# Performance work log

Measured on AMD Instinct MI355X. Metric: run time of the kernel, lower is better.

## Reference

```python
import jax, jax.numpy as jnp
import numpy as np
from jax import lax

B, L, DM, NL = 2, 1024, 768, 4
E = 2 * DM          # d_inner
N = 16              # d_state
K = 4               # d_conv
R = DM // 16        # dt_rank = 48


def setup_inputs() -> dict:
    key = jax.random.key(0)
    ks = jax.random.split(key, 16)
    s = 0.02
    x = jax.random.normal(ks[0], (B, L, DM), jnp.float32)
    boundary_prob = jax.random.uniform(ks[1], (B, L, 1), jnp.float32)
    in_proj_w = jax.random.normal(ks[2], (NL, 2 * E, DM), jnp.float32) * s
    conv_w = jax.random.normal(ks[3], (NL, E, K), jnp.float32) * 0.3
    conv_b = jax.random.normal(ks[4], (NL, E), jnp.float32) * 0.02
    x_proj_w = jax.random.normal(ks[5], (NL, R + 2 * N, E), jnp.float32) * s
    dt_proj_w = jax.random.normal(ks[6], (NL, E, R), jnp.float32) * (R ** -0.5)
    dt_proj_b = jax.random.uniform(ks[7], (NL, E), jnp.float32, -4.6, -3.0)
    A_log = jnp.log(jnp.broadcast_to(jnp.arange(1, N + 1, dtype=jnp.float32), (NL, E, N)))
    ssm_D = jnp.ones((NL, E), jnp.float32)
    out_proj_w = jax.random.normal(ks[8], (NL, DM, E), jnp.float32) * s
    ln_w = jnp.ones((NL, DM), jnp.float32)
    ln_b = jnp.zeros((NL, DM), jnp.float32)
    normf_w = jnp.ones((DM,), jnp.float32)
    normf_b = jnp.zeros((DM,), jnp.float32)
    ctrl_w1 = jax.random.normal(ks[9], (DM, DM + 1), jnp.float32) * s
    ctrl_b1 = jnp.zeros((DM,), jnp.float32)
    ctrl_w2 = jax.random.normal(ks[10], (DM, DM), jnp.float32) * s
    ctrl_b2 = jnp.zeros((DM,), jnp.float32)
    out_ln_w = jnp.ones((DM,), jnp.float32)
    out_ln_b = jnp.zeros((DM,), jnp.float32)
    return dict(x=x, boundary_prob=boundary_prob, in_proj_w=in_proj_w, conv_w=conv_w,
                conv_b=conv_b, x_proj_w=x_proj_w, dt_proj_w=dt_proj_w, dt_proj_b=dt_proj_b,
                A_log=A_log, ssm_D=ssm_D, out_proj_w=out_proj_w, ln_w=ln_w, ln_b=ln_b,
                normf_w=normf_w, normf_b=normf_b, ctrl_w1=ctrl_w1, ctrl_b1=ctrl_b1,
                ctrl_w2=ctrl_w2, ctrl_b2=ctrl_b2, out_ln_w=out_ln_w, out_ln_b=out_ln_b)


def _layernorm(h, w, b):
    m = h.mean(-1, keepdims=True)
    v = ((h - m) ** 2).mean(-1, keepdims=True)
    return (h - m) * lax.rsqrt(v + 1e-5) * w + b


def reference(x, boundary_prob, in_proj_w, conv_w, conv_b, x_proj_w, dt_proj_w, dt_proj_b,
              A_log, ssm_D, out_proj_w, ln_w, ln_b, normf_w, normf_b,
              ctrl_w1, ctrl_b1, ctrl_w2, ctrl_b2, out_ln_w, out_ln_b):
    bsz = x.shape[0]

    def mamba_layer(h, i):
        # in_proj (no bias): [B,L,DM] -> [B,L,2E]
        xz = jnp.einsum('bld,ed->ble', h, in_proj_w[i])
        xp, z = jnp.split(xz, 2, axis=-1)
        # causal depthwise conv1d (kernel K) + SiLU
        xc = xp.transpose(0, 2, 1)  # [B,E,L]
        xc = lax.conv_general_dilated(xc, conv_w[i][:, None, :], (1,), [(K - 1, 0)],
                                      feature_group_count=E,
                                      dimension_numbers=('NCH', 'OIH', 'NCH'))
        xc = jax.nn.silu(xc + conv_b[i][None, :, None]).transpose(0, 2, 1)  # [B,L,E]
        # x_proj -> dt, Bmat, Cmat
        dbl = jnp.einsum('ble,re->blr', xc, x_proj_w[i])
        dt, Bm, Cm = dbl[..., :R], dbl[..., R:R + N], dbl[..., R + N:]
        dt = jax.nn.softplus(jnp.einsum('blr,er->ble', dt, dt_proj_w[i]) + dt_proj_b[i])
        A = -jnp.exp(A_log[i])  # [E,N]

        def step(hstate, inp):
            xt, dtt, Bt, Ct = inp  # [B,E],[B,E],[B,N],[B,N]
            dA = jnp.exp(dtt[:, :, None] * A)                      # [B,E,N]
            hstate = dA * hstate + (dtt * xt)[:, :, None] * Bt[:, None, :]
            return hstate, jnp.einsum('ben,bn->be', hstate, Ct)

        h0 = jnp.zeros((bsz, E, N), x.dtype)
        _, ys = lax.scan(step, h0, (xc.swapaxes(0, 1), dt.swapaxes(0, 1),
                                    Bm.swapaxes(0, 1), Cm.swapaxes(0, 1)))
        y = ys.swapaxes(0, 1) + xc * ssm_D[i]
        y = y * jax.nn.silu(z)
        return jnp.einsum('ble,de->bld', y, out_proj_w[i])  # out_proj, no bias

    # Mamba Block stack: residual-in-fp32, pre-LayerNorm
    hs, residual = x, None
    for i in range(NL):
        residual = hs if residual is None else hs + residual
        hs = mamba_layer(_layernorm(residual, ln_w[i], ln_b[i]), i)
    residual = hs + residual
    mixed = _layernorm(residual, normf_w, normf_b)

    # boundary-controlled gate
    g_in = jnp.concatenate([x, boundary_prob], axis=-1)
    h1 = jax.nn.silu(g_in @ ctrl_w1.T + ctrl_b1)
    gate = jax.nn.sigmoid(h1 @ ctrl_w2.T + ctrl_b2)
    out = x + gate * (mixed - x)
    return _layernorm(out, out_ln_w, out_ln_b), gate
```

## Files before the change

### kernel.cpp

```cpp
#include <hip/hip_runtime.h>
#include <math.h>

static constexpr int B_  = 2;
static constexpr int L_  = 1024;
static constexpr int DM_ = 768;
static constexpr int NL_ = 4;
static constexpr int E_  = 2 * DM_;
static constexpr int N_  = 16;
static constexpr int K_  = 4;
static constexpr int R_  = DM_ / 16;
static constexpr int M_  = B_ * L_;
static constexpr int NC_ = 64;
static constexpr int T_  = L_ / NC_;
static constexpr int SK_ = 16;
static constexpr int KS_ = E_ / SK_;
static constexpr int OPK_ = 4;
static constexpr int NBE_ = N_ * B_ * E_;
static constexpr float LOG2E_ = 1.44269504088896340736f;

typedef __bf16 bf16x8 __attribute__((ext_vector_type(8)));
typedef __bf16 bf16x4 __attribute__((ext_vector_type(4)));
typedef short short8  __attribute__((ext_vector_type(8)));
typedef float f32x4   __attribute__((ext_vector_type(4)));

__device__ __forceinline__ short f2bf(float x) {
    __bf16 h = (__bf16)x;
    return __builtin_bit_cast(short, h);
}
__device__ __forceinline__ void st8(short* p, float4 x, float4 y) {
    short8 s;
    s[0] = f2bf(x.x); s[1] = f2bf(x.y); s[2] = f2bf(x.z); s[3] = f2bf(x.w);
    s[4] = f2bf(y.x); s[5] = f2bf(y.y); s[6] = f2bf(y.z); s[7] = f2bf(y.w);
    *(short8*)p = s;
}

__device__ __forceinline__ void gload16(const void* g, void* l) {
    __builtin_amdgcn_global_load_lds(
        (const __attribute__((address_space(1))) unsigned int*)g,
        (__attribute__((address_space(3))) unsigned int*)l,
        16, 0, 0);
}

__global__ __launch_bounds__(256) void gemm_bf16(
    const __bf16* __restrict__ A, int lda,
    const __bf16* __restrict__ W, int ldw,
    void* __restrict__ Cout, int ldc, int Kd, int out_bf16,
    const float* __restrict__ bias, int act,
    const float* __restrict__ u, const float* __restrict__ v, int vstride,
    void* __restrict__ Cout2, int splitN)
{
    constexpr int BM = 64;
    constexpr int BN = 64;
    constexpr int WN = 32;
    constexpr int FM = 2;
    constexpr int FN = 2;

    __shared__ __bf16 As[BM * 32];
    __shared__ __bf16 Bs[BN * 32];

    const int tid  = threadIdx.x;
    const int lane = tid & 63;
    const int wave = tid >> 6;
    const int wr = wave >> 1, wc = wave & 1;
    const int bm = blockIdx.y * BM;
    const int bn = blockIdx.x * BN;
    const int sk = blockIdx.z;

    A += (size_t)sk * Kd;
    W += (size_t)sk * Kd;
    const size_t cz = (size_t)sk * (size_t)gridDim.y * BM * ldc;

    const int sr = tid >> 2;
    const int sc = (tid & 3) << 3;
    const __bf16* ag0 = A + (size_t)(bm + sr) * lda + sc;
    const __bf16* wg0 = W + (size_t)(bn + sr) * ldw + sc;

    __bf16* lA0 = As + wave * 512;
    __bf16* lB0 = Bs + wave * 512;

    f32x4 acc[FM][FN];
#pragma unroll
    for (int i = 0; i < FM; ++i)
#pragma unroll
        for (int j = 0; j < FN; ++j)
            acc[i][j] = (f32x4){0.f, 0.f, 0.f, 0.f};

    const __bf16* ard = As + (wr * 32 + (lane & 15)) * 32 + ((lane >> 4) << 3);
    const __bf16* brd = Bs + (wc * 32 + (lane & 15)) * 32 + ((lane >> 4) << 3);

    const int NT = Kd / 32;
    for (int t = 0; t < NT; ++t) {
        const int k0 = t * 32;
        __syncthreads();
        gload16(ag0 + k0, lA0);
        gload16(wg0 + k0, lB0);
        __syncthreads();
        bf16x8 af[FM], bf[FN];
#pragma unroll
        for (int m = 0; m < FM; ++m)
            af[m] = *(const bf16x8*)(ard + m * 512);
#pragma unroll
        for (int n = 0; n < FN; ++n)
            bf[n] = *(const bf16x8*)(brd + n * 512);
#pragma unroll
        for (int m = 0; m < FM; ++m)
#pragma unroll
            for (int n = 0; n < FN; ++n)
                acc[m][n] = __builtin_amdgcn_mfma_f32_16x16x32_bf16(
                    af[m], bf[n], acc[m][n], 0, 0, 0);
    }

#pragma unroll
    for (int m = 0; m < FM; ++m) {
        const int row0 = bm + wr * 32 + m * 16 + ((lane >> 4) << 2);
#pragma unroll
        for (int n = 0; n < FN; ++n) {
            const int col = bn + wc * WN + n * 16 + (lane & 15);
            const float bia = bias ? bias[col] : 0.f;
            const float vv = u ? v[(size_t)col * vstride] : 0.f;
#pragma unroll
            for (int r = 0; r < 4; ++r) {
                float val = acc[m][n][r] + bia;
                if (Cout2) {
                    if (col < splitN) {
                        ((__bf16*)Cout)[(size_t)(row0 + r) * ldc + col] =
                            (__bf16)val;
                    } else {
                        float sv = val / (1.f + __expf(-val));
                        ((__bf16*)Cout2)[(size_t)(row0 + r) * ldc +
                                         (col - splitN)] = (__bf16)sv;
                    }
                    continue;
                }
                if (u) val += u[row0 + r] * vv;
                if (act == 1)      val = val / (1.f + __expf(-val));
                else if (act == 2) val = 1.f / (1.f + __expf(-val));
                else if (act == 3) val = (val > 20.f) ? val : log1pf(__expf(val));
                size_t off = cz + (size_t)(row0 + r) * ldc + col;
                if (out_bf16) ((__bf16*)Cout)[off] = (__bf16)val;
                else          ((float*)Cout)[off]  = val;
            }
        }
    }
}

__global__ __launch_bounds__(256) void cvt_bf16_kernel(
    const float* __restrict__ src, __bf16* __restrict__ dst, int n8)
{
    int i = blockIdx.x * 256 + threadIdx.x;
    if (i >= n8) return;
    const float4* s = (const float4*)src;
    st8((short*)(dst + (size_t)i * 8), s[2 * i], s[2 * i + 1]);
}

__global__ __launch_bounds__(256) void cvt_cw1_kernel(
    const float* __restrict__ src, __bf16* __restrict__ dst)
{
    int idx = blockIdx.x * 256 + threadIdx.x;
    if (idx >= DM_ * DM_) return;
    int r = idx / DM_, c = idx % DM_;
    dst[idx] = (__bf16)src[(size_t)r * (DM_ + 1) + c];
}

__global__ __launch_bounds__(256) void cvt_dpw_kernel(
    const float* __restrict__ src, __bf16* __restrict__ dst)
{
    int idx = blockIdx.x * 256 + threadIdx.x;
    if (idx >= NL_ * E_ * 64) return;
    int col = idx & 63;
    int row = idx >> 6;
    dst[idx] = (col < R_) ? (__bf16)src[(size_t)row * R_ + col] : (__bf16)0.f;
}

__global__ __launch_bounds__(256) void cvt_av_kernel(
    const float* __restrict__ alog, float* __restrict__ av)
{
    int idx = blockIdx.x * 256 + threadIdx.x;
    if (idx >= NL_ * E_ * N_) return;
    av[idx] = -__expf(alog[idx]) * LOG2E_;
}

__global__ __launch_bounds__(256) void xproj_mfma(
    const float* __restrict__ A, const float* __restrict__ W,
    float* __restrict__ part)
{
    constexpr int SA = 40;
    __shared__ short As[128 * SA];
    __shared__ short Ws[80 * SA];

    const int tid  = threadIdx.x;
    const int lane = tid & 63;
    const int wave = tid >> 6;
    const int sk = blockIdx.x;
    const int bm = blockIdx.y * 128;
    const int kbase = sk * KS_;

    const int ar = tid >> 1;
    const int ac = (tid & 1) << 4;
    const float* aptr = A + (size_t)(bm + ar) * E_ + kbase + ac;
    short* awr = &As[ar * SA + ac];

    const bool wact = tid < 160;
    const int wrow = tid >> 1;
    const float* wptr = W + (size_t)wrow * E_ + kbase + ac;
    short* wwr = &Ws[wrow * SA + ac];

    f32x4 acc[2][5];
#pragma unroll
    for (int i = 0; i < 2; ++i)
#pragma unroll
        for (int j = 0; j < 5; ++j)
            acc[i][j] = (f32x4){0.f, 0.f, 0.f, 0.f};

    const short* ard = &As[(wave * 32 + (lane & 15)) * SA + ((lane >> 4) << 3)];
    const short* brd = &Ws[(lane & 15) * SA + ((lane >> 4) << 3)];

    float4 aR[4], wR[4];
    auto loadT = [&](int k0) {
#pragma unroll
        for (int i = 0; i < 4; ++i)
            aR[i] = *(const float4*)(aptr + k0 + i * 4);
        if (wact) {
#pragma unroll
            for (int i = 0; i < 4; ++i)
                wR[i] = *(const float4*)(wptr + k0 + i * 4);
        }
    };

    constexpr int NT = KS_ / 32;
    loadT(0);
    for (int t = 0; t < NT; ++t) {
        __syncthreads();
        st8(awr, aR[0], aR[1]);
        st8(awr + 8, aR[2], aR[3]);
        if (wact) {
            st8(wwr, wR[0], wR[1]);
            st8(wwr + 8, wR[2], wR[3]);
        }
        __syncthreads();
        if (t + 1 < NT) loadT((t + 1) * 32);
        bf16x8 af[2], bf[5];
#pragma unroll
        for (int m = 0; m < 2; ++m)
            af[m] = *(const bf16x8*)(ard + m * 16 * SA);
#pragma unroll
        for (int n = 0; n < 5; ++n)
            bf[n] = *(const bf16x8*)(brd + n * 16 * SA);
#pragma unroll
        for (int m = 0; m < 2; ++m)
#pragma unroll
            for (int n = 0; n < 5; ++n)
                acc[m][n] = __builtin_amdgcn_mfma_f32_16x16x32_bf16(
                    af[m], bf[n], acc[m][n], 0, 0, 0);
    }

    float* pout = part + (size_t)sk * M_ * 80;
#pragma unroll
    for (int m = 0; m < 2; ++m) {
        const int row0 = bm + wave * 32 + m * 16 + ((lane >> 4) << 2);
#pragma unroll
        for (int n = 0; n < 5; ++n) {
            const int col = n * 16 + (lane & 15);
#pragma unroll
            for (int r = 0; r < 4; ++r)
                pout[(size_t)(row0 + r) * 80 + col] = acc[m][n][r];
        }
    }
}

__global__ __launch_bounds__(256) void xproj_reduce(
    const float* __restrict__ part, float* __restrict__ dbl,
    __bf16* __restrict__ dbl_bf)
{
    int idx = blockIdx.x * 256 + threadIdx.x;
    int m = idx / 80, col = idx % 80;
    float s = 0.f;
#pragma unroll
    for (int k = 0; k < SK_; ++k) s += part[(size_t)k * M_ * 80 + idx];
    dbl[idx] = s;
    if (col < R_)       dbl_bf[(size_t)m * 64 + col] = (__bf16)s;
    else if (col >= 64) dbl_bf[(size_t)m * 64 + (col - 16)] = (__bf16)0.f;
}

__device__ __forceinline__ float block_sum(float val, float* sm) {
#pragma unroll
    for (int o = 32; o > 0; o >>= 1) val += __shfl_down(val, o);
    int lane = threadIdx.x & 63, wid = threadIdx.x >> 6;
    __syncthreads();
    if (lane == 0) sm[wid] = val;
    __syncthreads();
    return sm[0] + sm[1] + sm[2] + sm[3];
}

__global__ __launch_bounds__(256) void add_ln_kernel(
    const float* __restrict__ src, int nparts,
    float* __restrict__ resid,
    const float* __restrict__ w, const float* __restrict__ b,
    float* __restrict__ outf, __bf16* __restrict__ outb, int do_add)
{
    constexpr int D = DM_;
    const size_t pstride = (size_t)M_ * DM_;
    const int row = blockIdx.x;
    const int tid = threadIdx.x;
    __shared__ float sm[4];
    const float* sp = src + (size_t)row * D;
    float* rp = resid + (size_t)row * D;

    float v[3];
    float s = 0.f;
#pragma unroll
    for (int j = 0; j < 3; ++j) {
        int d = j * 256 + tid;
        float vv = sp[d];
        for (int k = 1; k < nparts; ++k) vv += sp[(size_t)k * pstride + d];
        if (do_add) vv += rp[d];
        rp[d] = vv;
        v[j] = vv;
        s += vv;
    }
    float mean = block_sum(s, sm) * (1.f / D);
    float s2 = 0.f;
#pragma unroll
    for (int j = 0; j < 3; ++j) { float dlt = v[j] - mean; s2 += dlt * dlt; }
    float var = block_sum(s2, sm) * (1.f / D);
    float inv = rsqrtf(var + 1e-5f);
#pragma unroll
    for (int j = 0; j < 3; ++j) {
        int d = j * 256 + tid;
        float r = (v[j] - mean) * inv * w[d] + b[d];
        if (outf) outf[(size_t)row * D + d] = r;
        if (outb) outb[(size_t)row * D + d] = (__bf16)r;
    }
}

__device__ __forceinline__ float4 ld4bf(const __bf16* p) {
    bf16x4 v = *(const bf16x4*)p;
    return (float4){(float)v[0], (float)v[1], (float)v[2], (float)v[3]};
}

__global__ __launch_bounds__(256) void conv_silu_kernel(
    const __bf16* __restrict__ xp, const float* __restrict__ cw,
    const float* __restrict__ cb, float* __restrict__ xc)
{
    const int idx = blockIdx.x * 256 + threadIdx.x;
    if (idx >= M_ * E_ / 4) return;
    const int ec = (idx % (E_ / 4)) * 4;
    const int m  = idx / (E_ / 4);
    const int l  = m % L_;

    const float4 z4 = {0.f, 0.f, 0.f, 0.f};
    const __bf16* base = xp + (size_t)m * E_ + ec;
    float4 x0 = ld4bf(base);
    float4 x1 = (l >= 1) ? ld4bf(base - E_) : z4;
    float4 x2 = (l >= 2) ? ld4bf(base - 2 * E_) : z4;
    float4 x3 = (l >= 3) ? ld4bf(base - 3 * E_) : z4;
    const float4* wp = (const float4*)(cw + (size_t)ec * 4);
    float4 w0 = wp[0], w1 = wp[1], w2 = wp[2], w3 = wp[3];
    float4 bv = *(const float4*)(cb + ec);

    float4 o;
    o.x = bv.x + x3.x * w0.x + x2.x * w0.y + x1.x * w0.z + x0.x * w0.w;
    o.y = bv.y + x3.y * w1.x + x2.y * w1.y + x1.y * w1.z + x0.y * w1.w;
    o.z = bv.z + x3.z * w2.x + x2.z * w2.y + x1.z * w2.z + x0.z * w2.w;
    o.w = bv.w + x3.w * w3.x + x2.w * w3.y + x1.w * w3.z + x0.w * w3.w;
    o.x = o.x / (1.f + __expf(-o.x));
    o.y = o.y / (1.f + __expf(-o.y));
    o.z = o.z / (1.f + __expf(-o.z));
    o.w = o.w / (1.f + __expf(-o.w));
    *(float4*)(xc + (size_t)m * E_ + ec) = o;
}

__global__ __launch_bounds__(256) void scan_part1(
    const float* __restrict__ xc, const __bf16* __restrict__ dt,
    const float* __restrict__ dbl, const float* __restrict__ avl2,
    float* __restrict__ sumA, float* __restrict__ sumH)
{
    const int gid = blockIdx.x * 256 + threadIdx.x;
    const int c = gid % (B_ * E_);
    const int chunk = gid / (B_ * E_);
    const int b = c / E_;
    const int e = c % E_;

    float Av[N_];
    {
        const float4* Ap = (const float4*)(avl2 + e * N_);
        float4 A0 = Ap[0], A1 = Ap[1], A2 = Ap[2], A3 = Ap[3];
        float Ax[N_] = {A0.x, A0.y, A0.z, A0.w, A1.x, A1.y, A1.z, A1.w,
                        A2.x, A2.y, A2.z, A2.w, A3.x, A3.y, A3.z, A3.w};
#pragma unroll
        for (int n = 0; n < N_; ++n) Av[n] = Ax[n];
    }

    float h[N_];
#pragma unroll
    for (int n = 0; n < N_; ++n) h[n] = 0.f;
    float dts = 0.f;

    const size_t m0 = (size_t)b * L_ + (size_t)chunk * T_;
    for (int l = 0; l < T_; ++l) {
        size_t m = m0 + l;
        float dtv = (float)dt[m * E_ + e];
        float xv  = xc[m * E_ + e];
        float dtx = dtv * xv;
        const float4* Bp = (const float4*)(dbl + m * 80 + R_);
        float4 B0 = Bp[0], B1 = Bp[1], B2 = Bp[2], B3 = Bp[3];
        float Bv[N_] = {B0.x, B0.y, B0.z, B0.w, B1.x, B1.y, B1.z, B1.w,
                        B2.x, B2.y, B2.z, B2.w, B3.x, B3.y, B3.z, B3.w};
        dts += dtv;
#pragma unroll
        for (int n = 0; n < N_; ++n) {
            float dA = exp2f(dtv * Av[n]);
            h[n] = dA * h[n] + dtx * Bv[n];
        }
    }
#pragma unroll
    for (int n = 0; n < N_; ++n) {
        size_t o = (size_t)chunk * NBE_ + (size_t)n * (B_ * E_) + c;
        sumA[o] = exp2f(Av[n] * dts);
        sumH[o] = h[n];
    }
}

__global__ __launch_bounds__(256) void scan_part2(
    const float* __restrict__ sumA, float* __restrict__ sumH)
{
    const int idx = blockIdx.x * 256 + threadIdx.x;
    if (idx >= NBE_) return;
    float h = 0.f;
    for (int j = 0; j < NC_; j += 4) {
        size_t o0 = (size_t)(j + 0) * NBE_ + idx;
        size_t o1 = (size_t)(j + 1) * NBE_ + idx;
        size_t o2 = (size_t)(j + 2) * NBE_ + idx;
        size_t o3 = (size_t)(j + 3) * NBE_ + idx;
        float a0 = sumA[o0], a1 = sumA[o1], a2 = sumA[o2], a3 = sumA[o3];
        float h0 = sumH[o0], h1 = sumH[o1], h2 = sumH[o2], h3 = sumH[o3];
        sumH[o0] = h;  h = a0 * h + h0;
        sumH[o1] = h;  h = a1 * h + h1;
        sumH[o2] = h;  h = a2 * h + h2;
        sumH[o3] = h;  h = a3 * h + h3;
    }
}

__global__ __launch_bounds__(256) void scan_part3(
    const float* __restrict__ xc, const __bf16* __restrict__ dt,
    const float* __restrict__ dbl, const __bf16* __restrict__ siluz,
    const float* __restrict__ avl2, const float* __restrict__ ssm_D,
    const float* __restrict__ hstart, __bf16* __restrict__ y)
{
    const int gid = blockIdx.x * 256 + threadIdx.x;
    const int c = gid % (B_ * E_);
    const int chunk = gid / (B_ * E_);
    const int b = c / E_;
    const int e = c % E_;

    float Av[N_];
    {
        const float4* Ap = (const float4*)(avl2 + e * N_);
        float4 A0 = Ap[0], A1 = Ap[1], A2 = Ap[2], A3 = Ap[3];
        float Ax[N_] = {A0.x, A0.y, A0.z, A0.w, A1.x, A1.y, A1.z, A1.w,
                        A2.x, A2.y, A2.z, A2.w, A3.x, A3.y, A3.z, A3.w};
#pragma unroll
        for (int n = 0; n < N_; ++n) Av[n] = Ax[n];
    }
    const float Dv = ssm_D[e];

    float h[N_];
#pragma unroll
    for (int n = 0; n < N_; ++n)
        h[n] = hstart[(size_t)chunk * NBE_ + (size_t)n * (B_ * E_) + c];

    const size_t m0 = (size_t)b * L_ + (size_t)chunk * T_;
    for (int l = 0; l < T_; ++l) {
        size_t m = m0 + l;
        float dtv = (float)dt[m * E_ + e];
        float xv  = xc[m * E_ + e];
        float dtx = dtv * xv;
        const float4* Bp = (const float4*)(dbl + m * 80 + R_);
        float4 B0 = Bp[0], B1 = Bp[1], B2 = Bp[2], B3 = Bp[3];
        float4 C0 = Bp[4], C1 = Bp[5], C2 = Bp[6], C3 = Bp[7];
        float Bv[N_] = {B0.x, B0.y, B0.z, B0.w, B1.x, B1.y, B1.z, B1.w,
                        B2.x, B2.y, B2.z, B2.w, B3.x, B3.y, B3.z, B3.w};
        float Cv[N_] = {C0.x, C0.y, C0.z, C0.w, C1.x, C1.y, C1.z, C1.w,
                        C2.x, C2.y, C2.z, C2.w, C3.x, C3.y, C3.z, C3.w};
        float p = 0.f;
#pragma unroll
        for (int n = 0; n < N_; ++n) {
            float dA = exp2f(dtv * Av[n]);
            h[n] = dA * h[n] + dtx * Bv[n];
            p += h[n] * Cv[n];
        }
        float sz = (float)siluz[m * E_ + e];
        y[m * E_ + e] = (__bf16)((p + xv * Dv) * sz);
    }
}

__global__ __launch_bounds__(256) void final_out_kernel(
    const float* __restrict__ x, const float* __restrict__ gate,
    const float* __restrict__ mixed, const float* __restrict__ w,
    const float* __restrict__ b, float* __restrict__ outp)
{
    constexpr int D = DM_;
    const int row = blockIdx.x;
    const int tid = threadIdx.x;
    __shared__ float sm[4];
    const float* xp = x + (size_t)row * D;
    const float* gp = gate + (size_t)row * D;
    const float* mp = mixed + (size_t)row * D;

    float v[3];
    float s = 0.f;
#pragma unroll
    for (int j = 0; j < 3; ++j) {
        int d = j * 256 + tid;
        float xv = xp[d];
        float o = xv + gp[d] * (mp[d] - xv);
        v[j] = o;
        s += o;
    }
    float mean = block_sum(s, sm) * (1.f / D);
    float s2 = 0.f;
#pragma unroll
    for (int j = 0; j < 3; ++j) { float dlt = v[j] - mean; s2 += dlt * dlt; }
    float var = block_sum(s2, sm) * (1.f / D);
    float inv = rsqrtf(var + 1e-5f);
    float* op = outp + (size_t)row * D;
#pragma unroll
    for (int j = 0; j < 3; ++j) {
        int d = j * 256 + tid;
        op[d] = (v[j] - mean) * inv * w[d] + b[d];
    }
}

extern "C" void kernel_launch(void* const* d_in, const int* in_sizes, int n_in,
                              void* d_out, int out_size, void* d_ws, size_t ws_size,
                              hipStream_t stream)
{
    const float* x    = (const float*)d_in[0];
    const float* bp   = (const float*)d_in[1];
    const float* inw  = (const float*)d_in[2];
    const float* cw   = (const float*)d_in[3];
    const float* cb   = (const float*)d_in[4];
    const float* xpw  = (const float*)d_in[5];
    const float* dpw  = (const float*)d_in[6];
    const float* dpb  = (const float*)d_in[7];
    const float* alog = (const float*)d_in[8];
    const float* sD   = (const float*)d_in[9];
    const float* opw  = (const float*)d_in[10];
    const float* lnw  = (const float*)d_in[11];
    const float* lnb  = (const float*)d_in[12];
    const float* nfw  = (const float*)d_in[13];
    const float* nfb  = (const float*)d_in[14];
    const float* cw1  = (const float*)d_in[15];
    const float* cb1  = (const float*)d_in[16];
    const float* cw2  = (const float*)d_in[17];
    const float* cb2  = (const float*)d_in[18];
    const float* olnw = (const float*)d_in[19];
    const float* olnb = (const float*)d_in[20];
    float* out = (float*)d_out;

    float* p = (float*)d_ws;
    float* resid  = p;  p += (size_t)M_ * DM_;
    float* xcb    = p;  p += (size_t)M_ * E_;
    float* dblb   = p;  p += (size_t)M_ * 80;
    float* mixedf = p;  p += (size_t)M_ * DM_;
    float* sumA   = p;  p += (size_t)NC_ * NBE_;
    float* sumHst = p;  p += (size_t)NC_ * NBE_;
    float* part01 = p;  p += (size_t)OPK_ * M_ * DM_;
    float* xpart  = p;  p += (size_t)SK_ * M_ * 80;
    float* avl2   = p;  p += (size_t)NL_ * E_ * N_;
    __bf16* xp_bf  = (__bf16*)p; p += (size_t)M_ * E_ / 2;
    __bf16* y_bf   = (__bf16*)p; p += (size_t)M_ * E_ / 2;
    __bf16* z_bf   = (__bf16*)p; p += (size_t)M_ * E_ / 2;
    __bf16* dt_bf  = (__bf16*)p; p += (size_t)M_ * E_ / 2;
    __bf16* hln_bf = (__bf16*)p; p += (size_t)M_ * DM_ / 2;
    __bf16* dbl_bf = (__bf16*)p; p += (size_t)M_ * 64 / 2;
    __bf16* inw_bf = (__bf16*)p; p += (size_t)NL_ * 2 * E_ * DM_ / 2;
    __bf16* opw_bf = (__bf16*)p; p += (size_t)NL_ * DM_ * E_ / 2;
    __bf16* dpw_bf = (__bf16*)p; p += (size_t)NL_ * E_ * 64 / 2;
    __bf16* cw1b   = (__bf16*)p; p += (size_t)DM_ * DM_ / 2;
    __bf16* cw2b   = (__bf16*)p; p += (size_t)DM_ * DM_ / 2;
    __bf16* x_bf   = (__bf16*)p; p += (size_t)M_ * DM_ / 2;
    __bf16* h1_bf  = (__bf16*)p; p += (size_t)M_ * DM_ / 2;
    float* gate   = out + (size_t)M_ * DM_;

    cvt_bf16_kernel<<<(NL_ * 2 * E_ * DM_ / 8) / 256, 256, 0, stream>>>(
        inw, inw_bf, NL_ * 2 * E_ * DM_ / 8);
    cvt_bf16_kernel<<<(NL_ * DM_ * E_ / 8) / 256, 256, 0, stream>>>(
        opw, opw_bf, NL_ * DM_ * E_ / 8);
    cvt_cw1_kernel<<<(DM_ * DM_) / 256, 256, 0, stream>>>(cw1, cw1b);
    cvt_bf16_kernel<<<(DM_ * DM_ / 8 + 255) / 256, 256, 0, stream>>>(
        cw2, cw2b, DM_ * DM_ / 8);
    cvt_bf16_kernel<<<(M_ * DM_ / 8) / 256, 256, 0, stream>>>(
        x, x_bf, M_ * DM_ / 8);
    cvt_dpw_kernel<<<(NL_ * E_ * 64) / 256, 256, 0, stream>>>(dpw, dpw_bf);
    cvt_av_kernel<<<(NL_ * E_ * N_) / 256, 256, 0, stream>>>(alog, avl2);

    for (int i = 0; i < NL_; ++i) {
        if (i == 0)
            add_ln_kernel<<<M_, 256, 0, stream>>>(x, 1, resid,
                lnw, lnb, nullptr, hln_bf, 0);
        else
            add_ln_kernel<<<M_, 256, 0, stream>>>(part01, OPK_, resid,
                lnw + i * DM_, lnb + i * DM_, nullptr, hln_bf, 1);
        gemm_bf16<<<dim3(2 * E_ / 64, M_ / 64, 1), 256, 0, stream>>>(
            hln_bf, DM_, inw_bf + (size_t)i * 2 * E_ * DM_, DM_, xp_bf, E_,
            DM_, 0, nullptr, 0, nullptr, nullptr, 0, z_bf, E_);
        conv_silu_kernel<<<(M_ * E_ / 4) / 256, 256, 0, stream>>>(
            xp_bf, cw + (size_t)i * E_ * K_, cb + (size_t)i * E_, xcb);
        xproj_mfma<<<dim3(SK_, M_ / 128), 256, 0, stream>>>(
            xcb, xpw + (size_t)i * 80 * E_, xpart);
        xproj_reduce<<<(M_ * 80) / 256, 256, 0, stream>>>(xpart, dblb, dbl_bf);
        gemm_bf16<<<dim3(E_ / 64, M_ / 64, 1), 256, 0, stream>>>(
            dbl_bf, 64, dpw_bf + (size_t)i * E_ * 64, 64, dt_bf, E_,
            64, 1, dpb + (size_t)i * E_, 3, nullptr, nullptr, 0, nullptr, 0);
        scan_part1<<<(NC_ * B_ * E_) / 256, 256, 0, stream>>>(
            xcb, dt_bf, dblb, avl2 + (size_t)i * E_ * N_, sumA, sumHst);
        scan_part2<<<(NBE_) / 256, 256, 0, stream>>>(sumA, sumHst);
        scan_part3<<<(NC_ * B_ * E_) / 256, 256, 0, stream>>>(
            xcb, dt_bf, dblb, z_bf, avl2 + (size_t)i * E_ * N_,
            sD + (size_t)i * E_, sumHst, y_bf);
        gemm_bf16<<<dim3(DM_ / 64, M_ / 64, OPK_), 256, 0, stream>>>(
            y_bf, E_, opw_bf + (size_t)i * DM_ * E_, E_, part01, DM_,
            E_ / OPK_, 0, nullptr, 0, nullptr, nullptr, 0, nullptr, 0);
    }

    add_ln_kernel<<<M_, 256, 0, stream>>>(part01, OPK_, resid,
        nfw, nfb, mixedf, nullptr, 1);
    gemm_bf16<<<dim3(DM_ / 64, M_ / 64, 1), 256, 0, stream>>>(
        x_bf, DM_, cw1b, DM_, h1_bf, DM_, DM_, 1,
        cb1, 1, bp, cw1 + DM_, DM_ + 1, nullptr, 0);
    gemm_bf16<<<dim3(DM_ / 64, M_ / 64, 1), 256, 0, stream>>>(
        h1_bf, DM_, cw2b, DM_, gate, DM_, DM_, 0,
        cb2, 2, nullptr, nullptr, 0, nullptr, 0);
    final_out_kernel<<<M_, 256, 0, stream>>>(x, gate, mixedf, olnw, olnb, out);
}
```

Measured before the change: 659.6 us.

## Store conv output in bf16 and route x_proj through shared bf16 GEMM

The conv+SiLU output now goes to a bf16 buffer instead of fp32, which halves the traffic for the x_proj GEMM and both scan passes that read it. The custom xproj_mfma kernel is removed. x_proj now runs through the generic split-K gemm_bf16, using x_proj weights converted once to bf16 and zero-padded from 80 to 128 rows. The out_proj split-K factor also drops from 4 to 2. In exchange, padding adds wasted compute and partial-sum traffic, xc loses precision, and the lower split-K may reduce parallelism.

Result: no change. 663.5 us (+0.6%).

```diff
diff --git a/kernel.cpp b/kernel.cpp
--- a/kernel.cpp
+++ b/kernel.cpp
@@ -14,7 +14,8 @@
 static constexpr int T_  = L_ / NC_;
 static constexpr int SK_ = 16;
 static constexpr int KS_ = E_ / SK_;
-static constexpr int OPK_ = 4;
+static constexpr int XPN_ = 128;
+static constexpr int OPK_ = 2;
 static constexpr int NBE_ = N_ * B_ * E_;
 static constexpr float LOG2E_ = 1.44269504088896340736f;
 
@@ -172,6 +173,18 @@
     dst[idx] = (col < R_) ? (__bf16)src[(size_t)row * R_ + col] : (__bf16)0.f;
 }
 
+__global__ __launch_bounds__(256) void cvt_xpw_kernel(
+    const float* __restrict__ src, __bf16* __restrict__ dst)
+{
+    int idx = blockIdx.x * 256 + threadIdx.x;
+    if (idx >= NL_ * XPN_ * E_) return;
+    int col = idx % E_;
+    int rr  = (idx / E_) % XPN_;
+    int lay = idx / (XPN_ * E_);
+    dst[idx] = (rr < 80)
+        ? (__bf16)src[((size_t)lay * 80 + rr) * E_ + col] : (__bf16)0.f;
+}
+
 __global__ __launch_bounds__(256) void cvt_av_kernel(
     const float* __restrict__ alog, float* __restrict__ av)
 {
@@ -180,94 +193,6 @@
     av[idx] = -__expf(alog[idx]) * LOG2E_;
 }
 
-__global__ __launch_bounds__(256) void xproj_mfma(
-    const float* __restrict__ A, const float* __restrict__ W,
-    float* __restrict__ part)
-{
-    constexpr int SA = 40;
-    __shared__ short As[128 * SA];
-    __shared__ short Ws[80 * SA];
-
-    const int tid  = threadIdx.x;
-    const int lane = tid & 63;
-    const int wave = tid >> 6;
-    const int sk = blockIdx.x;
-    const int bm = blockIdx.y * 128;
-    const int kbase = sk * KS_;
-
-    const int ar = tid >> 1;
-    const int ac = (tid & 1) << 4;
-    const float* aptr = A + (size_t)(bm + ar) * E_ + kbase + ac;
-    short* awr = &As[ar * SA + ac];
-
-    const bool wact = tid < 160;
-    const int wrow = tid >> 1;
-    const float* wptr = W + (size_t)wrow * E_ + kbase + ac;
-    short* wwr = &Ws[wrow * SA + ac];
-
-    f32x4 acc[2][5];
-#pragma unroll
-    for (int i = 0; i < 2; ++i)
-#pragma unroll
-        for (int j = 0; j < 5; ++j)
-            acc[i][j] = (f32x4){0.f, 0.f, 0.f, 0.f};
-
-    const short* ard = &As[(wave * 32 + (lane & 15)) * SA + ((lane >> 4) << 3)];
-    const short* brd = &Ws[(lane & 15) * SA + ((lane >> 4) << 3)];
-
-    float4 aR[4], wR[4];
-    auto loadT = [&](int k0) {
-#pragma unroll
-        for (int i = 0; i < 4; ++i)
-            aR[i] = *(const float4*)(aptr + k0 + i * 4);
-        if (wact) {
-#pragma unroll
-            for (int i = 0; i < 4; ++i)
-                wR[i] = *(const float4*)(wptr + k0 + i * 4);
-        }
-    };
-
-    constexpr int NT = KS_ / 32;
-    loadT(0);
-    for (int t = 0; t < NT; ++t) {
-        __syncthreads();
-        st8(awr, aR[0], aR[1]);
-        st8(awr + 8, aR[2], aR[3]);
-        if (wact) {
-            st8(wwr, wR[0], wR[1]);
-            st8(wwr + 8, wR[2], wR[3]);
-        }
-        __syncthreads();
-        if (t + 1 < NT) loadT((t + 1) * 32);
-        bf16x8 af[2], bf[5];
-#pragma unroll
-        for (int m = 0; m < 2; ++m)
-            af[m] = *(const bf16x8*)(ard + m * 16 * SA);
-#pragma unroll
-        for (int n = 0; n < 5; ++n)
-            bf[n] = *(const bf16x8*)(brd + n * 16 * SA);
-#pragma unroll
-        for (int m = 0; m < 2; ++m)
-#pragma unroll
-            for (int n = 0; n < 5; ++n)
-                acc[m][n] = __builtin_amdgcn_mfma_f32_16x16x32_bf16(
-                    af[m], bf[n], acc[m][n], 0, 0, 0);
-    }
-
-    float* pout = part + (size_t)sk * M_ * 80;
-#pragma unroll
-    for (int m = 0; m < 2; ++m) {
-        const int row0 = bm + wave * 32 + m * 16 + ((lane >> 4) << 2);
-#pragma unroll
-        for (int n = 0; n < 5; ++n) {
-            const int col = n * 16 + (lane & 15);
-#pragma unroll
-            for (int r = 0; r < 4; ++r)
-                pout[(size_t)(row0 + r) * 80 + col] = acc[m][n][r];
-        }
-    }
-}
-
 __global__ __launch_bounds__(256) void xproj_reduce(
     const float* __restrict__ part, float* __restrict__ dbl,
     __bf16* __restrict__ dbl_bf)
@@ -276,7 +201,8 @@
     int m = idx / 80, col = idx % 80;
     float s = 0.f;
 #pragma unroll
-    for (int k = 0; k < SK_; ++k) s += part[(size_t)k * M_ * 80 + idx];
+    for (int k = 0; k < SK_; ++k)
+        s += part[(size_t)k * M_ * XPN_ + (size_t)m * XPN_ + col];
     dbl[idx] = s;
     if (col < R_)       dbl_bf[(size_t)m * 64 + col] = (__bf16)s;
     else if (col >= 64) dbl_bf[(size_t)m * 64 + (col - 16)] = (__bf16)0.f;
@@ -340,7 +266,7 @@
 
 __global__ __launch_bounds__(256) void conv_silu_kernel(
     const __bf16* __restrict__ xp, const float* __restrict__ cw,
-    const float* __restrict__ cb, float* __restrict__ xc)
+    const float* __restrict__ cb, __bf16* __restrict__ xc)
 {
     const int idx = blockIdx.x * 256 + threadIdx.x;
     if (idx >= M_ * E_ / 4) return;
@@ -363,15 +289,16 @@
     o.y = bv.y + x3.y * w1.x + x2.y * w1.y + x1.y * w1.z + x0.y * w1.w;
     o.z = bv.z + x3.z * w2.x + x2.z * w2.y + x1.z * w2.z + x0.z * w2.w;
     o.w = bv.w + x3.w * w3.x + x2.w * w3.y + x1.w * w3.z + x0.w * w3.w;
-    o.x = o.x / (1.f + __expf(-o.x));
-    o.y = o.y / (1.f + __expf(-o.y));
-    o.z = o.z / (1.f + __expf(-o.z));
-    o.w = o.w / (1.f + __expf(-o.w));
-    *(float4*)(xc + (size_t)m * E_ + ec) = o;
+    bf16x4 ov;
+    ov[0] = (__bf16)(o.x / (1.f + __expf(-o.x)));
+    ov[1] = (__bf16)(o.y / (1.f + __expf(-o.y)));
+    ov[2] = (__bf16)(o.z / (1.f + __expf(-o.z)));
+    ov[3] = (__bf16)(o.w / (1.f + __expf(-o.w)));
+    *(bf16x4*)(xc + (size_t)m * E_ + ec) = ov;
 }
 
 __global__ __launch_bounds__(256) void scan_part1(
-    const float* __restrict__ xc, const __bf16* __restrict__ dt,
+    const __bf16* __restrict__ xc, const __bf16* __restrict__ dt,
     const float* __restrict__ dbl, const float* __restrict__ avl2,
     float* __restrict__ sumA, float* __restrict__ sumH)
 {
@@ -400,7 +327,7 @@
     for (int l = 0; l < T_; ++l) {
         size_t m = m0 + l;
         float dtv = (float)dt[m * E_ + e];
-        float xv  = xc[m * E_ + e];
+        float xv  = (float)xc[m * E_ + e];
         float dtx = dtv * xv;
         const float4* Bp = (const float4*)(dbl + m * 80 + R_);
         float4 B0 = Bp[0], B1 = Bp[1], B2 = Bp[2], B3 = Bp[3];
@@ -442,7 +369,7 @@
 }
 
 __global__ __launch_bounds__(256) void scan_part3(
-    const float* __restrict__ xc, const __bf16* __restrict__ dt,
+    const __bf16* __restrict__ xc, const __bf16* __restrict__ dt,
     const float* __restrict__ dbl, const __bf16* __restrict__ siluz,
     const float* __restrict__ avl2, const float* __restrict__ ssm_D,
     const float* __restrict__ hstart, __bf16* __restrict__ y)
@@ -473,7 +400,7 @@
     for (int l = 0; l < T_; ++l) {
         size_t m = m0 + l;
         float dtv = (float)dt[m * E_ + e];
-        float xv  = xc[m * E_ + e];
+        float xv  = (float)xc[m * E_ + e];
         float dtx = dtv * xv;
         const float4* Bp = (const float4*)(dbl + m * 80 + R_);
         float4 B0 = Bp[0], B1 = Bp[1], B2 = Bp[2], B3 = Bp[3];
@@ -560,15 +487,15 @@
 
     float* p = (float*)d_ws;
     float* resid  = p;  p += (size_t)M_ * DM_;
-    float* xcb    = p;  p += (size_t)M_ * E_;
     float* dblb   = p;  p += (size_t)M_ * 80;
     float* mixedf = p;  p += (size_t)M_ * DM_;
     float* sumA   = p;  p += (size_t)NC_ * NBE_;
     float* sumHst = p;  p += (size_t)NC_ * NBE_;
     float* part01 = p;  p += (size_t)OPK_ * M_ * DM_;
-    float* xpart  = p;  p += (size_t)SK_ * M_ * 80;
+    float* xpart  = p;  p += (size_t)SK_ * M_ * XPN_;
     float* avl2   = p;  p += (size_t)NL_ * E_ * N_;
     __bf16* xp_bf  = (__bf16*)p; p += (size_t)M_ * E_ / 2;
+    __bf16* xc_bf  = (__bf16*)p; p += (size_t)M_ * E_ / 2;
     __bf16* y_bf   = (__bf16*)p; p += (size_t)M_ * E_ / 2;
     __bf16* z_bf   = (__bf16*)p; p += (size_t)M_ * E_ / 2;
     __bf16* dt_bf  = (__bf16*)p; p += (size_t)M_ * E_ / 2;
@@ -577,6 +504,7 @@
     __bf16* inw_bf = (__bf16*)p; p += (size_t)NL_ * 2 * E_ * DM_ / 2;
     __bf16* opw_bf = (__bf16*)p; p += (size_t)NL_ * DM_ * E_ / 2;
     __bf16* dpw_bf = (__bf16*)p; p += (size_t)NL_ * E_ * 64 / 2;
+    __bf16* xpw_bf = (__bf16*)p; p += (size_t)NL_ * XPN_ * E_ / 2;
     __bf16* cw1b   = (__bf16*)p; p += (size_t)DM_ * DM_ / 2;
     __bf16* cw2b   = (__bf16*)p; p += (size_t)DM_ * DM_ / 2;
     __bf16* x_bf   = (__bf16*)p; p += (size_t)M_ * DM_ / 2;
@@ -593,6 +521,7 @@
     cvt_bf16_kernel<<<(M_ * DM_ / 8) / 256, 256, 0, stream>>>(
         x, x_bf, M_ * DM_ / 8);
     cvt_dpw_kernel<<<(NL_ * E_ * 64) / 256, 256, 0, stream>>>(dpw, dpw_bf);
+    cvt_xpw_kernel<<<(NL_ * XPN_ * E_) / 256, 256, 0, stream>>>(xpw, xpw_bf);
     cvt_av_kernel<<<(NL_ * E_ * N_) / 256, 256, 0, stream>>>(alog, avl2);
 
     for (int i = 0; i < NL_; ++i) {
@@ -606,18 +535,19 @@
             hln_bf, DM_, inw_bf + (size_t)i * 2 * E_ * DM_, DM_, xp_bf, E_,
             DM_, 0, nullptr, 0, nullptr, nullptr, 0, z_bf, E_);
         conv_silu_kernel<<<(M_ * E_ / 4) / 256, 256, 0, stream>>>(
-            xp_bf, cw + (size_t)i * E_ * K_, cb + (size_t)i * E_, xcb);
-        xproj_mfma<<<dim3(SK_, M_ / 128), 256, 0, stream>>>(
-            xcb, xpw + (size_t)i * 80 * E_, xpart);
+            xp_bf, cw + (size_t)i * E_ * K_, cb + (size_t)i * E_, xc_bf);
+        gemm_bf16<<<dim3(XPN_ / 64, M_ / 64, SK_), 256, 0, stream>>>(
+            xc_bf, E_, xpw_bf + (size_t)i * XPN_ * E_, E_, xpart, XPN_,
+            KS_, 0, nullptr, 0, nullptr, nullptr, 0, nullptr, 0);
         xproj_reduce<<<(M_ * 80) / 256, 256, 0, stream>>>(xpart, dblb, dbl_bf);
         gemm_bf16<<<dim3(E_ / 64, M_ / 64, 1), 256, 0, stream>>>(
             dbl_bf, 64, dpw_bf + (size_t)i * E_ * 64, 64, dt_bf, E_,
             64, 1, dpb + (size_t)i * E_, 3, nullptr, nullptr, 0, nullptr, 0);
         scan_part1<<<(NC_ * B_ * E_) / 256, 256, 0, stream>>>(
-            xcb, dt_bf, dblb, avl2 + (size_t)i * E_ * N_, sumA, sumHst);
+            xc_bf, dt_bf, dblb, avl2 + (size_t)i * E_ * N_, sumA, sumHst);
         scan_part2<<<(NBE_) / 256, 256, 0, stream>>>(sumA, sumHst);
         scan_part3<<<(NC_ * B_ * E_) / 256, 256, 0, stream>>>(
-            xcb, dt_bf, dblb, z_bf, avl2 + (size_t)i * E_ * N_,
+            xc_bf, dt_bf, dblb, z_bf, avl2 + (size_t)i * E_ * N_,
             sD + (size_t)i * E_, sumHst, y_bf);
         gemm_bf16<<<dim3(DM_ / 64, M_ / 64, OPK_), 256, 0, stream>>>(
             y_bf, E_, opw_bf + (size_t)i * DM_ * E_, E_, part01, DM_,
```
